# Kernel optimization log

Hardware: AMD Instinct MI355X
Metric: run time of the kernel (lower is better)

The kernel has to match this reference:

```python
import jax, jax.numpy as jnp
import numpy as np

GROUPS = 32
EPS = 1e-5


def group_norm(x, gamma, beta):
    # x: [B,H,W,C], channels_last, groups over channel dim (Keras GroupNormalization default)
    B, H, W, C = x.shape
    xg = x.reshape(B, H, W, GROUPS, C // GROUPS)
    mean = xg.mean(axis=(1, 2, 4), keepdims=True)
    var = xg.var(axis=(1, 2, 4), keepdims=True)
    xn = ((xg - mean) * jax.lax.rsqrt(var + EPS)).reshape(B, H, W, C)
    return xn * gamma + beta


def conv1x1(x, w, b):
    # 1x1 conv == per-pixel dense: [B,H,W,C] x [C,D] -> [B,H,W,D]
    return jnp.einsum('bhwc,cd->bhwd', x, w) + b


def setup_inputs() -> dict:
    key = jax.random.key(0)
    ks = jax.random.split(key, 10)
    C = 512
    s = 1.0 / np.sqrt(C)
    inp = {
        'x': jax.random.normal(ks[0], (2, 64, 64, C), dtype=jnp.float32),
        'gamma': jnp.ones((C,), jnp.float32),
        'beta': jnp.zeros((C,), jnp.float32),
        'wq': jax.random.normal(ks[1], (C, C), jnp.float32) * s,
        'bq': jnp.zeros((C,), jnp.float32),
        'wk': jax.random.normal(ks[2], (C, C), jnp.float32) * s,
        'bk': jnp.zeros((C,), jnp.float32),
        'wv': jax.random.normal(ks[3], (C, C), jnp.float32) * s,
        'bv': jnp.zeros((C,), jnp.float32),
        'wp': jax.random.normal(ks[4], (C, C), jnp.float32) * s,
        'bp': jnp.zeros((C,), jnp.float32),
    }
    return inp


def reference(x, gamma, beta, wq, bq, wk, bk, wv, bv, wp, bp):
    B, H, W, C = x.shape
    N = H * W
    xn = group_norm(x, gamma, beta)
    q = conv1x1(xn, wq, bq).reshape(B, N, C)
    k = conv1x1(xn, wk, bk).reshape(B, N, C)
    v = conv1x1(xn, wv, bv).reshape(B, N, C)
    scale = 1.0 / jnp.sqrt(jnp.asarray(C, x.dtype))
    scores = jnp.einsum('bnc,bmc->bnm', q, k) * scale  # [B,N,N]
    attn = jax.nn.softmax(scores, axis=-1)
    out = jnp.einsum('bnm,bmc->bnc', attn, v).reshape(B, H, W, C)
    return conv1x1(out, wp, bp) + x
```

## Files before the change

kernel.cpp:

```cpp
#include <hip/hip_runtime.h>
#include <hip/hip_fp16.h>

typedef _Float16 half_t;
typedef _Float16 half8 __attribute__((ext_vector_type(8)));
typedef float floatx4 __attribute__((ext_vector_type(4)));

static constexpr int BATCH = 2;
static constexpr int NSP = 4096;
static constexpr int CH = 512;
static constexpr int NQKV = 3 * CH;

static constexpr size_t OFF_STATS = 0;
static constexpr size_t OFF_ROWSUM = 512;
static constexpr size_t OFF_WQKV = 36864;
static constexpr size_t WQKV_BYTES = (size_t)NQKV * CH * 2;
static constexpr size_t OFF_WP = OFF_WQKV + WQKV_BYTES;
static constexpr size_t WP_BYTES = (size_t)CH * CH * 2;
static constexpr size_t OFF_XN = OFF_WP + WP_BYTES;
static constexpr size_t XN_BYTES = (size_t)BATCH * NSP * CH * 2;
static constexpr size_t OFF_QKV = OFF_XN + XN_BYTES;
static constexpr size_t QKV_BYTES = (size_t)BATCH * NSP * NQKV * 2;
static constexpr size_t OFF_VT = OFF_QKV + QKV_BYTES;
static constexpr size_t OFF_AO = OFF_VT + XN_BYTES;
static constexpr size_t OFF_S = OFF_AO + XN_BYTES;
static constexpr size_t S_BYTES_1 = (size_t)NSP * NSP * 2;

__device__ __forceinline__ void gld16(void* lds, const void* g) {
  __builtin_amdgcn_global_load_lds(
      (__attribute__((address_space(1))) void*)(g),
      (__attribute__((address_space(3))) void*)(lds),
      16, 0, 0);
}

__global__ void zero4(floatx4* p, long n4) {
  long i = (long)blockIdx.x * 256 + threadIdx.x;
  if (i < n4) p[i] = floatx4{0.f, 0.f, 0.f, 0.f};
}

__global__ __launch_bounds__(256) void gn_stats(const float* __restrict__ x,
                                                float* __restrict__ st) {
  int b = blockIdx.y;
  int tid = (int)threadIdx.x;
  int c0 = (tid * 4) & (CH - 1);
  int g = c0 >> 4;
  const float* base = x + (long)b * NSP * CH + (long)blockIdx.x * 16 * CH + tid * 4;
  float s = 0.f, s2 = 0.f;
#pragma unroll
  for (int it = 0; it < 8; ++it) {
    floatx4 v = *(const floatx4*)(base + (long)it * 1024);
#pragma unroll
    for (int r = 0; r < 4; ++r) { s += v[r]; s2 += v[r] * v[r]; }
  }
  __shared__ float gs[32], gs2[32];
  if (tid < 32) { gs[tid] = 0.f; gs2[tid] = 0.f; }
  __syncthreads();
  atomicAdd(&gs[g], s);
  atomicAdd(&gs2[g], s2);
  __syncthreads();
  if (tid < 32) {
    atomicAdd(&st[(b * 32 + tid) * 2], gs[tid]);
    atomicAdd(&st[(b * 32 + tid) * 2 + 1], gs2[tid]);
  }
}

__global__ void gn_finalize(float* st) {
  int bg = threadIdx.x;
  float s = st[bg * 2], s2 = st[bg * 2 + 1];
  const float inv = 1.f / 65536.f;
  float mean = s * inv;
  float var = s2 * inv - mean * mean;
  st[bg * 2] = mean;
  st[bg * 2 + 1] = rsqrtf(var + 1e-5f);
}

__global__ __launch_bounds__(256) void gn_apply(const float* __restrict__ x,
                                                const float* __restrict__ st,
                                                const float* __restrict__ gamma,
                                                const float* __restrict__ beta,
                                                half_t* __restrict__ xn) {
  long i = ((long)blockIdx.x * 256 + threadIdx.x) * 8;
  int c = (int)(i & (CH - 1));
  int b = (int)(i >> 21);
  int g = c >> 4;
  float mean = st[((b << 5) + g) * 2];
  float rstd = st[((b << 5) + g) * 2 + 1];
  floatx4 a = *(const floatx4*)(x + i);
  floatx4 d = *(const floatx4*)(x + i + 4);
  half8 o;
#pragma unroll
  for (int r = 0; r < 4; ++r) {
    o[r]     = (half_t)((a[r] - mean) * rstd * gamma[c + r] + beta[c + r]);
    o[r + 4] = (half_t)((d[r] - mean) * rstd * gamma[c + r + 4] + beta[c + r + 4]);
  }
  *(half8*)(xn + i) = o;
}

__global__ __launch_bounds__(256) void transpose_w(
    const float* __restrict__ w0, const float* __restrict__ w1,
    const float* __restrict__ w2, const float* __restrict__ w3,
    half_t* __restrict__ o0, half_t* __restrict__ o1,
    half_t* __restrict__ o2, half_t* __restrict__ o3) {
  const float* w; half_t* o;
  switch (blockIdx.z) {
    case 0: w = w0; o = o0; break;
    case 1: w = w1; o = o1; break;
    case 2: w = w2; o = o2; break;
    default: w = w3; o = o3; break;
  }
  __shared__ float t[32][33];
  int d0 = blockIdx.x * 32, c0 = blockIdx.y * 32;
  int tx = threadIdx.x & 31, ty = threadIdx.x >> 5;
#pragma unroll
  for (int i = 0; i < 4; ++i)
    t[ty + i * 8][tx] = w[(long)(c0 + ty + i * 8) * CH + d0 + tx];
  __syncthreads();
#pragma unroll
  for (int i = 0; i < 4; ++i) {
    int d = ty + i * 8;
    o[(long)(d0 + d) * CH + c0 + tx] = (half_t)t[tx][d];
  }
}

__global__ __launch_bounds__(256) void transpose_v(const half_t* __restrict__ v,
                                                   half_t* __restrict__ vt) {
  __shared__ half_t t[32][33];
  int b = blockIdx.z;
  int d0 = blockIdx.x * 32, n0 = blockIdx.y * 32;
  int tx = threadIdx.x & 31, ty = threadIdx.x >> 5;
  const half_t* vb = v + (long)b * NSP * NQKV;
  half_t* ob = vt + (long)b * NSP * CH;
#pragma unroll
  for (int i = 0; i < 4; ++i)
    t[ty + i * 8][tx] = vb[(long)(n0 + ty + i * 8) * NQKV + d0 + tx];
  __syncthreads();
#pragma unroll
  for (int i = 0; i < 4; ++i) {
    int d = ty + i * 8;
    ob[(long)(d0 + d) * NSP + n0 + tx] = t[tx][d];
  }
}

template <int BM, int BN, int BK, int EPI, int SWZ, typename OutT>
__global__ __launch_bounds__(256) void gemm_nt(
    const half_t* __restrict__ X, const half_t* __restrict__ Y,
    OutT* __restrict__ Co, const float* __restrict__ b0,
    const float* __restrict__ b1, const float* __restrict__ b2,
    const float* __restrict__ resid, float* __restrict__ rowsum,
    int M, int N, int K, int ldx, int ldy, int ldc,
    long xbs, long ybs, long cbs, float scale) {
  constexpr int SM = BM / 32;
  constexpr int SN = BN / 32;
  constexpr int ROWS = BM + BN;
  constexpr int CPR = BK / 8;
  constexpr int RPW = 64 / CPR;
  constexpr int ROUNDS = (ROWS * BK * 2) / 4096;
  constexpr int KSTEPS = BK / 32;
  static_assert(BM % (4 * RPW) == 0, "no As/Bs straddle within a round");
  __shared__ __align__(16) half_t Sh[ROWS * BK];

  const int zb = blockIdx.z;
  int bx, by;
  if (SWZ) {
    int lin = (int)(blockIdx.x + gridDim.x * blockIdx.y);
    int wmt = 256 / (int)gridDim.x;
    by = wmt * (lin >> 8) + ((lin & 255) % wmt);
    bx = (lin & 255) / wmt;
  } else {
    bx = blockIdx.x;
    by = blockIdx.y;
  }

  const half_t* Xb = X + (long)zb * xbs;
  const half_t* Yb = Y + (long)zb * ybs;
  OutT* Cb = Co + (long)zb * cbs;

  const int m0 = by * BM;
  const int n0 = bx * BN;
  const int tid = (int)threadIdx.x;
  const int wave = tid >> 6;
  const int lane = tid & 63;
  const int quad = lane >> 4;
  const int l16 = lane & 15;
  const int wm = wave >> 1;
  const int wn = wave & 1;

  floatx4 acc[SM][SN] = {};

  const int srow = lane / CPR;
  const int schunk = lane % CPR;
  const char* Xc = (const char*)Xb;

  int soff[ROUNDS];
#pragma unroll
  for (int r = 0; r < ROUNDS; ++r) {
    int row = r * (4 * RPW) + wave * RPW + srow;
    int gchunk = schunk ^ (row & (CPR - 1));
    const char* p = (row < BM)
        ? (const char*)(Xb + (long)(m0 + row) * ldx)
        : (const char*)(Yb + (long)(n0 + row - BM) * ldy);
    soff[r] = (int)(p + gchunk * 16 - Xc);
  }

  int offA[SM], offB[SN];
#pragma unroll
  for (int i = 0; i < SM; ++i) {
    int m = wm * (BM / 2) + i * 16 + l16;
    int cc = quad ^ (m & (CPR - 1));
    offA[i] = (m * BK + cc * 8) * 2;
  }
#pragma unroll
  for (int j = 0; j < SN; ++j) {
    int n = wn * (BN / 2) + j * 16 + l16;
    int cc = quad ^ (n & (CPR - 1));
    offB[j] = (BM * BK + n * BK + cc * 8) * 2;
  }

  for (int k0 = 0; k0 < K; k0 += BK) {
#pragma unroll
    for (int r = 0; r < ROUNDS; ++r) {
      gld16((char*)Sh + (r * 4 + wave) * 1024, Xc + (long)soff[r]);
      soff[r] += BK * 2;
    }
    __syncthreads();

#pragma unroll
    for (int kk = 0; kk < KSTEPS; ++kk) {
      const int kx = kk << 6;
      half8 af[SM], bf[SN];
#pragma unroll
      for (int i = 0; i < SM; ++i)
        af[i] = *(const half8*)((const char*)Sh + (offA[i] ^ kx));
#pragma unroll
      for (int j = 0; j < SN; ++j)
        bf[j] = *(const half8*)((const char*)Sh + (offB[j] ^ kx));
#pragma unroll
      for (int i = 0; i < SM; ++i)
#pragma unroll
        for (int j = 0; j < SN; ++j)
          acc[i][j] = __builtin_amdgcn_mfma_f32_16x16x32_f16(af[i], bf[j], acc[i][j], 0, 0, 0);
    }
    __syncthreads();
  }

#pragma unroll
  for (int i = 0; i < SM; ++i) {
    int gmb = m0 + wm * (BM / 2) + i * 16 + quad * 4;
    float rs[4] = {0.f, 0.f, 0.f, 0.f};
    float inv[4];
    if (EPI == 4) {
#pragma unroll
      for (int r = 0; r < 4; ++r)
        inv[r] = 1.f / rowsum[(long)zb * NSP + gmb + r];
    }
#pragma unroll
    for (int j = 0; j < SN; ++j) {
      int gn = n0 + wn * (BN / 2) + j * 16 + l16;
      float bias = 0.f, sc = 1.f;
      if (EPI == 1) {
        if (gn < CH) { bias = b0[gn]; sc = scale; }
        else if (gn < 2 * CH) { bias = b1[gn - CH]; }
        else { bias = b2[gn - 2 * CH]; }
      } else if (EPI == 2) {
        bias = b0[gn];
      }
#pragma unroll
      for (int r = 0; r < 4; ++r) {
        long idx = (long)(gmb + r) * ldc + gn;
        float v = acc[i][j][r];
        if (EPI == 1) v = (v + bias) * sc;
        if (EPI == 2) v = v + bias + resid[idx];
        if (EPI == 3) { v = __expf(v); rs[r] += v; }
        if (EPI == 4) v *= inv[r];
        Cb[idx] = (OutT)v;
      }
    }
    if (EPI == 3) {
#pragma unroll
      for (int r = 0; r < 4; ++r) {
        float v = rs[r];
        v += __shfl_xor(v, 1);
        v += __shfl_xor(v, 2);
        v += __shfl_xor(v, 4);
        v += __shfl_xor(v, 8);
        if (l16 == 0) atomicAdd(&rowsum[(long)zb * NSP + gmb + r], v);
      }
    }
  }
}

extern "C" void kernel_launch(void* const* d_in, const int* in_sizes, int n_in,
                              void* d_out, int out_size, void* d_ws, size_t ws_size,
                              hipStream_t stream) {
  const float* x = (const float*)d_in[0];
  const float* gamma = (const float*)d_in[1];
  const float* beta = (const float*)d_in[2];
  const float* wq = (const float*)d_in[3];
  const float* bq = (const float*)d_in[4];
  const float* wk = (const float*)d_in[5];
  const float* bk = (const float*)d_in[6];
  const float* wv = (const float*)d_in[7];
  const float* bv = (const float*)d_in[8];
  const float* wp = (const float*)d_in[9];
  const float* bp = (const float*)d_in[10];
  float* out = (float*)d_out;
  char* ws = (char*)d_ws;

  float* st = (float*)(ws + OFF_STATS);
  float* rsum = (float*)(ws + OFF_ROWSUM);
  half_t* wqkvT = (half_t*)(ws + OFF_WQKV);
  half_t* wpT = (half_t*)(ws + OFF_WP);
  half_t* xn = (half_t*)(ws + OFF_XN);
  half_t* qkv = (half_t*)(ws + OFF_QKV);
  half_t* vt = (half_t*)(ws + OFF_VT);
  half_t* ao = (half_t*)(ws + OFF_AO);
  half_t* S = (half_t*)(ws + OFF_S);

  half_t* q = qkv;
  half_t* k = qkv + CH;
  half_t* v = qkv + 2 * CH;

  const float scale = 0.044194173824159216f;
  const long bQKV = (long)NSP * NQKV;
  const long bNC = (long)NSP * CH;
  const long bNN = (long)NSP * NSP;

  zero4<<<9, 256, 0, stream>>>((floatx4*)st, 2080);
  gn_stats<<<dim3(256, BATCH), 256, 0, stream>>>(x, st);
  gn_finalize<<<1, 64, 0, stream>>>(st);
  gn_apply<<<2048, 256, 0, stream>>>(x, st, gamma, beta, xn);
  transpose_w<<<dim3(16, 16, 4), 256, 0, stream>>>(
      wq, wk, wv, wp, wqkvT, wqkvT + (size_t)CH * CH, wqkvT + 2 * (size_t)CH * CH, wpT);

  gemm_nt<128, 128, 64, 1, 0, half_t><<<dim3(NQKV / 128, BATCH * NSP / 128, 1), 256, 0, stream>>>(
      xn, wqkvT, qkv, bq, bk, bv, nullptr, nullptr, BATCH * NSP, NQKV, CH,
      CH, CH, NQKV, 0, 0, 0, scale);
  transpose_v<<<dim3(16, 128, BATCH), 256, 0, stream>>>(v, vt);

  bool full = ws_size >= OFF_S + 2 * S_BYTES_1;
  if (full) {
    gemm_nt<128, 128, 64, 3, 1, half_t><<<dim3(32, 32, BATCH), 256, 0, stream>>>(
        q, k, S, nullptr, nullptr, nullptr, nullptr, rsum, NSP, NSP, CH,
        NQKV, NQKV, NSP, bQKV, bQKV, bNN, 1.f);
    gemm_nt<64, 64, 128, 4, 1, half_t><<<dim3(CH / 64, NSP / 64, BATCH), 256, 0, stream>>>(
        S, vt, ao, nullptr, nullptr, nullptr, nullptr, rsum, NSP, CH, NSP,
        NSP, NSP, CH, bNN, bNC, bNC, 1.f);
  } else {
    for (int bb = 0; bb < BATCH; ++bb) {
      gemm_nt<128, 128, 64, 3, 1, half_t><<<dim3(32, 32, 1), 256, 0, stream>>>(
          q + bb * bQKV, k + bb * bQKV, S, nullptr, nullptr, nullptr, nullptr,
          rsum + bb * NSP, NSP, NSP, CH, NQKV, NQKV, NSP, 0, 0, 0, 1.f);
      gemm_nt<64, 64, 128, 4, 1, half_t><<<dim3(CH / 64, NSP / 64, 1), 256, 0, stream>>>(
          S, vt + bb * bNC, ao + bb * bNC, nullptr, nullptr, nullptr, nullptr,
          rsum + bb * NSP, NSP, CH, NSP, NSP, NSP, CH, 0, 0, 0, 1.f);
    }
  }
  gemm_nt<64, 64, 128, 2, 0, float><<<dim3(CH / 64, BATCH * NSP / 64, 1), 256, 0, stream>>>(
      ao, wpT, out, bp, nullptr, nullptr, x, nullptr, BATCH * NSP, CH, CH,
      CH, CH, CH, 0, 0, 0, 1.f);
}
```

Before: 276.3 us.

## Split-K the attention-value GEMM with larger tiles and a combine kernel

New measurement: 262.7 us. 4.9% less time.

```diff
diff --git a/kernel.cpp b/kernel.cpp
--- a/kernel.cpp
+++ b/kernel.cpp
@@ -9,10 +9,12 @@
 static constexpr int NSP = 4096;
 static constexpr int CH = 512;
 static constexpr int NQKV = 3 * CH;
+static constexpr int KSPLIT = 4;
 
 static constexpr size_t OFF_STATS = 0;
 static constexpr size_t OFF_ROWSUM = 512;
-static constexpr size_t OFF_WQKV = 36864;
+static constexpr size_t OFF_PST = 33280;
+static constexpr size_t OFF_WQKV = 196608;
 static constexpr size_t WQKV_BYTES = (size_t)NQKV * CH * 2;
 static constexpr size_t OFF_WP = OFF_WQKV + WQKV_BYTES;
 static constexpr size_t WP_BYTES = (size_t)CH * CH * 2;
@@ -24,6 +26,7 @@
 static constexpr size_t OFF_AO = OFF_VT + XN_BYTES;
 static constexpr size_t OFF_S = OFF_AO + XN_BYTES;
 static constexpr size_t S_BYTES_1 = (size_t)NSP * NSP * 2;
+static constexpr size_t OFF_PART = OFF_XN;
 
 __device__ __forceinline__ void gld16(void* lds, const void* g) {
   __builtin_amdgcn_global_load_lds(
@@ -32,17 +35,11 @@
       16, 0, 0);
 }
 
-__global__ void zero4(floatx4* p, long n4) {
-  long i = (long)blockIdx.x * 256 + threadIdx.x;
-  if (i < n4) p[i] = floatx4{0.f, 0.f, 0.f, 0.f};
-}
-
 __global__ __launch_bounds__(256) void gn_stats(const float* __restrict__ x,
-                                                float* __restrict__ st) {
+                                                float* __restrict__ pst) {
   int b = blockIdx.y;
   int tid = (int)threadIdx.x;
-  int c0 = (tid * 4) & (CH - 1);
-  int g = c0 >> 4;
+  int g = ((tid * 4) & (CH - 1)) >> 4;
   const float* base = x + (long)b * NSP * CH + (long)blockIdx.x * 16 * CH + tid * 4;
   float s = 0.f, s2 = 0.f;
 #pragma unroll
@@ -58,19 +55,43 @@
   atomicAdd(&gs2[g], s2);
   __syncthreads();
   if (tid < 32) {
-    atomicAdd(&st[(b * 32 + tid) * 2], gs[tid]);
-    atomicAdd(&st[(b * 32 + tid) * 2 + 1], gs2[tid]);
-  }
-}
-
-__global__ void gn_finalize(float* st) {
-  int bg = threadIdx.x;
-  float s = st[bg * 2], s2 = st[bg * 2 + 1];
-  const float inv = 1.f / 65536.f;
-  float mean = s * inv;
-  float var = s2 * inv - mean * mean;
-  st[bg * 2] = mean;
-  st[bg * 2 + 1] = rsqrtf(var + 1e-5f);
+    long idx = ((long)(b * 256 + blockIdx.x) * 32 + tid) * 2;
+    pst[idx] = gs[tid];
+    pst[idx + 1] = gs2[tid];
+  }
+}
+
+__global__ __launch_bounds__(256) void gn_finalize(const float* __restrict__ pst,
+                                                   float* __restrict__ st,
+                                                   float* __restrict__ rowsum) {
+  int tid = (int)threadIdx.x;
+  int bg = tid & 63;
+  int p = tid >> 6;
+  int b = bg >> 5, g = bg & 31;
+  float s = 0.f, s2 = 0.f;
+  for (int j = 0; j < 64; ++j) {
+    int chunk = p * 64 + j;
+    long idx = ((long)(b * 256 + chunk) * 32 + g) * 2;
+    s += pst[idx];
+    s2 += pst[idx + 1];
+  }
+  __shared__ float rs[64][4], rs2[64][4];
+  rs[bg][p] = s;
+  rs2[bg][p] = s2;
+  __syncthreads();
+  if (tid < 64) {
+    float ts = rs[tid][0] + rs[tid][1] + rs[tid][2] + rs[tid][3];
+    float ts2 = rs2[tid][0] + rs2[tid][1] + rs2[tid][2] + rs2[tid][3];
+    const float inv = 1.f / 65536.f;
+    float mean = ts * inv;
+    float var = ts2 * inv - mean * mean;
+    st[tid * 2] = mean;
+    st[tid * 2 + 1] = rsqrtf(var + 1e-5f);
+  }
+  floatx4* rz = (floatx4*)rowsum;
+#pragma unroll
+  for (int j = 0; j < 8; ++j)
+    rz[tid + j * 256] = floatx4{0.f, 0.f, 0.f, 0.f};
 }
 
 __global__ __launch_bounds__(256) void gn_apply(const float* __restrict__ x,
@@ -140,7 +161,7 @@
   }
 }
 
-template <int BM, int BN, int BK, int EPI, int SWZ, typename OutT>
+template <int BM, int BN, int BK, int EPI, int SWZ, int KSP, typename OutT>
 __global__ __launch_bounds__(256) void gemm_nt(
     const half_t* __restrict__ X, const half_t* __restrict__ Y,
     OutT* __restrict__ Co, const float* __restrict__ b0,
@@ -158,21 +179,25 @@
   static_assert(BM % (4 * RPW) == 0, "no As/Bs straddle within a round");
   __shared__ __align__(16) half_t Sh[ROWS * BK];
 
-  const int zb = blockIdx.z;
+  const int zb = blockIdx.z / KSP;
+  const int ks = blockIdx.z % KSP;
   int bx, by;
-  if (SWZ) {
+  if (SWZ == 1) {
     int lin = (int)(blockIdx.x + gridDim.x * blockIdx.y);
     int wmt = 256 / (int)gridDim.x;
     by = wmt * (lin >> 8) + ((lin & 255) % wmt);
     bx = (lin & 255) / wmt;
+  } else if (SWZ == 2) {
+    by = blockIdx.x;
+    bx = blockIdx.y;
   } else {
     bx = blockIdx.x;
     by = blockIdx.y;
   }
 
-  const half_t* Xb = X + (long)zb * xbs;
-  const half_t* Yb = Y + (long)zb * ybs;
-  OutT* Cb = Co + (long)zb * cbs;
+  const half_t* Xb = X + (long)zb * xbs + (long)ks * K;
+  const half_t* Yb = Y + (long)zb * ybs + (long)ks * K;
+  OutT* Cb = Co + (long)blockIdx.z * cbs;
 
   const int m0 = by * BM;
   const int n0 = bx * BN;
@@ -246,12 +271,6 @@
   for (int i = 0; i < SM; ++i) {
     int gmb = m0 + wm * (BM / 2) + i * 16 + quad * 4;
     float rs[4] = {0.f, 0.f, 0.f, 0.f};
-    float inv[4];
-    if (EPI == 4) {
-#pragma unroll
-      for (int r = 0; r < 4; ++r)
-        inv[r] = 1.f / rowsum[(long)zb * NSP + gmb + r];
-    }
 #pragma unroll
     for (int j = 0; j < SN; ++j) {
       int gn = n0 + wn * (BN / 2) + j * 16 + l16;
@@ -270,7 +289,6 @@
         if (EPI == 1) v = (v + bias) * sc;
         if (EPI == 2) v = v + bias + resid[idx];
         if (EPI == 3) { v = __expf(v); rs[r] += v; }
-        if (EPI == 4) v *= inv[r];
         Cb[idx] = (OutT)v;
       }
     }
@@ -286,6 +304,27 @@
       }
     }
   }
+}
+
+__global__ __launch_bounds__(256) void pv_combine(const half_t* __restrict__ part,
+                                                  const float* __restrict__ rowsum,
+                                                  half_t* __restrict__ ao) {
+  const long bNC = (long)NSP * CH;
+  long i = ((long)blockIdx.x * 256 + threadIdx.x) * 8;
+  int b = (int)(i >> 21);
+  long inner = i & ((1L << 21) - 1);
+  float inv = 1.f / rowsum[i >> 9];
+  float s[8] = {};
+#pragma unroll
+  for (int ks = 0; ks < KSPLIT; ++ks) {
+    half8 h = *(const half8*)(part + ((long)(b * KSPLIT + ks)) * bNC + inner);
+#pragma unroll
+    for (int r = 0; r < 8; ++r) s[r] += (float)h[r];
+  }
+  half8 o;
+#pragma unroll
+  for (int r = 0; r < 8; ++r) o[r] = (half_t)(s[r] * inv);
+  *(half8*)(ao + i) = o;
 }
 
 extern "C" void kernel_launch(void* const* d_in, const int* in_sizes, int n_in,
@@ -307,6 +346,7 @@
 
   float* st = (float*)(ws + OFF_STATS);
   float* rsum = (float*)(ws + OFF_ROWSUM);
+  float* pst = (float*)(ws + OFF_PST);
   half_t* wqkvT = (half_t*)(ws + OFF_WQKV);
   half_t* wpT = (half_t*)(ws + OFF_WP);
   half_t* xn = (half_t*)(ws + OFF_XN);
@@ -314,6 +354,7 @@
   half_t* vt = (half_t*)(ws + OFF_VT);
   half_t* ao = (half_t*)(ws + OFF_AO);
   half_t* S = (half_t*)(ws + OFF_S);
+  half_t* part = (half_t*)(ws + OFF_PART);
 
   half_t* q = qkv;
   half_t* k = qkv + CH;
@@ -324,37 +365,38 @@
   const long bNC = (long)NSP * CH;
   const long bNN = (long)NSP * NSP;
 
-  zero4<<<9, 256, 0, stream>>>((floatx4*)st, 2080);
-  gn_stats<<<dim3(256, BATCH), 256, 0, stream>>>(x, st);
-  gn_finalize<<<1, 64, 0, stream>>>(st);
+  gn_stats<<<dim3(256, BATCH), 256, 0, stream>>>(x, pst);
+  gn_finalize<<<1, 256, 0, stream>>>(pst, st, rsum);
   gn_apply<<<2048, 256, 0, stream>>>(x, st, gamma, beta, xn);
   transpose_w<<<dim3(16, 16, 4), 256, 0, stream>>>(
       wq, wk, wv, wp, wqkvT, wqkvT + (size_t)CH * CH, wqkvT + 2 * (size_t)CH * CH, wpT);
 
-  gemm_nt<128, 128, 64, 1, 0, half_t><<<dim3(NQKV / 128, BATCH * NSP / 128, 1), 256, 0, stream>>>(
+  gemm_nt<128, 128, 64, 1, 2, 1, half_t><<<dim3(BATCH * NSP / 128, NQKV / 128, 1), 256, 0, stream>>>(
       xn, wqkvT, qkv, bq, bk, bv, nullptr, nullptr, BATCH * NSP, NQKV, CH,
       CH, CH, NQKV, 0, 0, 0, scale);
   transpose_v<<<dim3(16, 128, BATCH), 256, 0, stream>>>(v, vt);
 
   bool full = ws_size >= OFF_S + 2 * S_BYTES_1;
   if (full) {
-    gemm_nt<128, 128, 64, 3, 1, half_t><<<dim3(32, 32, BATCH), 256, 0, stream>>>(
+    gemm_nt<128, 128, 64, 3, 1, 1, half_t><<<dim3(32, 32, BATCH), 256, 0, stream>>>(
         q, k, S, nullptr, nullptr, nullptr, nullptr, rsum, NSP, NSP, CH,
         NQKV, NQKV, NSP, bQKV, bQKV, bNN, 1.f);
-    gemm_nt<64, 64, 128, 4, 1, half_t><<<dim3(CH / 64, NSP / 64, BATCH), 256, 0, stream>>>(
-        S, vt, ao, nullptr, nullptr, nullptr, nullptr, rsum, NSP, CH, NSP,
+    gemm_nt<128, 128, 64, 0, 2, KSPLIT, half_t><<<dim3(NSP / 128, CH / 128, BATCH * KSPLIT), 256, 0, stream>>>(
+        S, vt, part, nullptr, nullptr, nullptr, nullptr, nullptr, NSP, CH, NSP / KSPLIT,
         NSP, NSP, CH, bNN, bNC, bNC, 1.f);
+    pv_combine<<<2048, 256, 0, stream>>>(part, rsum, ao);
   } else {
     for (int bb = 0; bb < BATCH; ++bb) {
-      gemm_nt<128, 128, 64, 3, 1, half_t><<<dim3(32, 32, 1), 256, 0, stream>>>(
+      gemm_nt<128, 128, 64, 3, 1, 1, half_t><<<dim3(32, 32, 1), 256, 0, stream>>>(
           q + bb * bQKV, k + bb * bQKV, S, nullptr, nullptr, nullptr, nullptr,
           rsum + bb * NSP, NSP, NSP, CH, NQKV, NQKV, NSP, 0, 0, 0, 1.f);
-      gemm_nt<64, 64, 128, 4, 1, half_t><<<dim3(CH / 64, NSP / 64, 1), 256, 0, stream>>>(
-          S, vt + bb * bNC, ao + bb * bNC, nullptr, nullptr, nullptr, nullptr,
-          rsum + bb * NSP, NSP, CH, NSP, NSP, NSP, CH, 0, 0, 0, 1.f);
+      gemm_nt<128, 128, 64, 0, 2, KSPLIT, half_t><<<dim3(NSP / 128, CH / 128, KSPLIT), 256, 0, stream>>>(
+          S, vt + bb * bNC, part + (long)bb * KSPLIT * bNC, nullptr, nullptr, nullptr,
+          nullptr, nullptr, NSP, CH, NSP / KSPLIT, NSP, NSP, CH, 0, 0, bNC, 1.f);
     }
-  }
-  gemm_nt<64, 64, 128, 2, 0, float><<<dim3(CH / 64, BATCH * NSP / 64, 1), 256, 0, stream>>>(
+    pv_combine<<<2048, 256, 0, stream>>>(part, rsum, ao);
+  }
+  gemm_nt<64, 64, 128, 2, 2, 1, float><<<dim3(BATCH * NSP / 64, CH / 64, 1), 256, 0, stream>>>(
       ao, wpT, out, bp, nullptr, nullptr, x, nullptr, BATCH * NSP, CH, CH,
       CH, CH, CH, 0, 0, 0, 1.f);
 }
```
